# Kernel tuning notes

Measured on AMD Instinct MI355X. Metric: run time of the kernel, lower is better.

## Reference

```python
import jax, jax.numpy as jnp
import numpy as np
import math

_KX = np.array([[1., 0., -1.], [2., 0., -2.], [1., 0., -1.]], dtype=np.float32)
_SOBEL = np.stack([_KX, _KX.T])[:, None]  # (2,1,3,3): gx, gy
_SCALES = [16, 8, 4, 2, 1]
_NBINS = 9


def _hog_layer(x, pw, pb, pool):
    # x: (B,1,H,W); reflect-pad 3x3 Sobel conv -> (B,2,H,W)
    xp = jnp.pad(x, ((0, 0), (0, 0), (1, 1), (1, 1)), mode='reflect')
    gxy = jax.lax.conv_general_dilated(
        xp, jnp.asarray(_SOBEL), (1, 1), 'VALID',
        dimension_numbers=('NCHW', 'OIHW', 'NCHW'))
    gx, gy = gxy[:, 0], gxy[:, 1]
    mag = jnp.sqrt(gx * gx + gy * gy)                       # (B,H,W)
    phase = jnp.arctan2(gx, gy)
    bins = (jnp.floor(phase / math.pi * _NBINS) % _NBINS).astype(jnp.int32)
    # one-hot scatter of magnitude into orientation bins (matches scatter_ on dim 1)
    out = jax.nn.one_hot(bins, _NBINS, dtype=mag.dtype) * mag[..., None]  # (B,H,W,9)
    out = jnp.transpose(out, (0, 3, 1, 2))                  # (B,9,H,W)
    # 1x1 conv with stride=pool == strided slice + channel mix
    o = out[:, :, ::pool, ::pool]
    h = jnp.einsum('oc,nchw->nohw', pw, o) + pb[None, :, None, None]
    nrm = jnp.linalg.norm(h, axis=1, keepdims=True)
    return h / jnp.maximum(nrm, 1e-12)                      # F.normalize(p=2, dim=1)


def _hog_rgb(imgs, pw, pb, pool):
    # run the (shared) HOG layer on R,G,B independently, concat on channel dim
    N, C, H, W = imgs.shape
    h = _hog_layer(imgs.reshape(N * C, 1, H, W), pw, pb, pool)
    return h.reshape(N, C * _NBINS, h.shape[2], h.shape[3])  # (N,27,H/s,W/s)


def _recal_mask(mask, s):
    B, H, W = mask.shape[0], mask.shape[2], mask.shape[3]
    m = mask.astype(jnp.float32).reshape(B, H // s, s, W // s, s)
    return jnp.transpose(m, (0, 1, 3, 2, 4)).mean((-2, -1))  # (B,H/s,W/s)


def _loss(preds, imgs, mask, pws, pbs):
    loss = jnp.float32(0.0)
    for k, s in enumerate(_SCALES):
        tgt = _hog_rgb(imgs, pws[k], pbs[k], s)
        M = _recal_mask(mask, s)
        loss = loss + (((preds[k] - tgt) ** 2).mean(axis=1) * M).sum() / M.sum()
    return loss


def setup_inputs() -> dict:
    key = jax.random.key(0)
    ks = jax.random.split(key, 20)
    N, H, W = 32, 224, 224
    d = {}
    d['imgs'] = jax.random.normal(ks[0], (N, 3, H, W), dtype=jnp.float32)
    d['mask'] = jax.random.uniform(ks[1], (N, 1, H, W), dtype=jnp.float32)
    for k, s in enumerate(_SCALES):
        d['pred%d' % k] = jax.random.normal(ks[2 + k], (N, 27, H // s, W // s), dtype=jnp.float32)
        d['pw%d' % k] = jax.random.normal(ks[7 + k], (9, 9), dtype=jnp.float32) / 3.0
        d['pb%d' % k] = jax.random.normal(ks[12 + k], (9,), dtype=jnp.float32) / 3.0
    return d


def reference(imgs, mask, pred0, pred1, pred2, pred3, pred4,
              pw0, pw1, pw2, pw3, pw4, pb0, pb1, pb2, pb3, pb4):
    preds = [pred0, pred1, pred2, pred3, pred4]
    pws = [pw0, pw1, pw2, pw3, pw4]
    pbs = [pb0, pb1, pb2, pb3, pb4]
    return _loss(preds, imgs, mask, pws, pbs)
```

## Files before the change

kernel.cpp:

```cpp
#include <hip/hip_runtime.h>

#define N_IMG 32
#define H_IMG 224
#define W_IMG 224

#define BS16_END 25
#define BS8_END 123
#define BS4_END 515
#define BS2_END 2083
#define NBLK_TOTAL 8355

__device__ __forceinline__ int reflect_idx(int i, int n) {
    if (i < 0) return -i;
    if (i >= n) return 2 * n - 2 - i;
    return i;
}

__device__ __forceinline__ int bin_from_g(float gx, float gy) {
    float u = gx * __builtin_copysignf(1.0f, gy);
    float w = __builtin_fabsf(gy);
    const float T[9] = {-5.6712818f, -1.7320508f, -0.83909963f, -0.36397023f,
                        0.0f, 0.36397023f, 0.83909963f, 1.7320508f, 5.6712818f};
    int c = 0;
    #pragma unroll
    for (int k = 0; k < 9; ++k) c += (u >= T[k] * w) ? 1 : 0;
    int b = c + 4;
    return (b >= 9) ? b - 9 : b;
}

template <int S>
__device__ __forceinline__ void scale_body(int rel_bid,
    const float* __restrict__ imgs, const float* __restrict__ mask,
    const float* __restrict__ pred,
    const float* spwT, const float* spb, const float* sA, const float* sB,
    float Cc, float& local, float& mlocal)
{
    constexpr int Hs = H_IMG / S, Ws = W_IMG / S;
    int vt = rel_bid * 256 + (int)threadIdx.x;
    if (vt >= N_IMG * Hs * Ws) return;
    int j = vt % Ws;
    int t = vt / Ws;
    int i = t % Hs;
    int n = t / Hs;

    float M;
    const float* mbase = mask + (size_t)n * H_IMG * W_IMG + (size_t)(i * S) * W_IMG + j * S;
    if constexpr (S == 1) {
        M = mbase[0];
    } else if constexpr (S == 2) {
        float2 a = *(const float2*)(mbase);
        float2 b = *(const float2*)(mbase + W_IMG);
        M = (a.x + a.y + b.x + b.y) * 0.25f;
    } else {
        float msum = 0.0f;
        #pragma unroll
        for (int a = 0; a < S; ++a) {
            const float* mr = mbase + (size_t)a * W_IMG;
            #pragma unroll
            for (int q = 0; q < S / 4; ++q) {
                float4 fv = *(const float4*)(mr + q * 4);
                msum += (fv.x + fv.y) + (fv.z + fv.w);
            }
        }
        M = msum * (1.0f / (float)(S * S));
    }

    int y = i * S, x = j * S;
    int y0 = reflect_idx(y - 1, H_IMG), y2 = reflect_idx(y + 1, H_IMG);
    int x0 = reflect_idx(x - 1, W_IMG), x2 = reflect_idx(x + 1, W_IMG);
    constexpr size_t cstride = (size_t)Hs * Ws;

    float d2 = 0.0f;
    #pragma unroll
    for (int c = 0; c < 3; ++c) {
        const float* im = imgs + (size_t)(n * 3 + c) * H_IMG * W_IMG;
        const float* q0 = im + (size_t)y0 * W_IMG;
        const float* q1 = im + (size_t)y  * W_IMG;
        const float* q2 = im + (size_t)y2 * W_IMG;
        float p00 = q0[x0], p01 = q0[x], p02 = q0[x2];
        float p10 = q1[x0],             p12 = q1[x2];
        float p20 = q2[x0], p21 = q2[x], p22 = q2[x2];

        const float* pr = pred + ((size_t)(n * 27 + c * 9) * Hs + i) * Ws + j;
        float p[9];
        #pragma unroll
        for (int o = 0; o < 9; ++o) p[o] = pr[o * cstride];

        float gx = (p00 - p02) + 2.0f * (p10 - p12) + (p20 - p22);
        float gy = (p00 - p20) + 2.0f * (p01 - p21) + (p02 - p22);
        float mag = sqrtf(gx * gx + gy * gy);
        int bn = bin_from_g(gx, gy);
        float nrm2 = fmaf(mag, fmaf(mag, sA[bn], 2.0f * sB[bn]), Cc);
        float inv = 1.0f / fmaxf(sqrtf(nrm2), 1e-12f);

        #pragma unroll
        for (int o = 0; o < 9; ++o) {
            float h = fmaf(spwT[bn * 9 + o], mag, spb[o]) * inv;
            float dd = p[o] - h;
            d2 += dd * dd;
        }
    }

    local = M * d2 * (1.0f / 27.0f);
    if constexpr (S == 1) mlocal = M;
}

__global__ void __launch_bounds__(256) fused_kernel(
    const float* __restrict__ imgs, const float* __restrict__ mask,
    const float* __restrict__ pred0, const float* __restrict__ pred1,
    const float* __restrict__ pred2, const float* __restrict__ pred3,
    const float* __restrict__ pred4,
    const float* __restrict__ pw0, const float* __restrict__ pw1,
    const float* __restrict__ pw2, const float* __restrict__ pw3,
    const float* __restrict__ pw4,
    const float* __restrict__ pb0, const float* __restrict__ pb1,
    const float* __restrict__ pb2, const float* __restrict__ pb3,
    const float* __restrict__ pb4,
    double* __restrict__ pl, double* __restrict__ pm)
{
    __shared__ float spwT[81];
    __shared__ float spb[9];
    __shared__ float sA[9], sB[9], sC[1];

    int bid = blockIdx.x;
    const float* pw;  const float* pb;
    if (bid < BS16_END)      { pw = pw0; pb = pb0; }
    else if (bid < BS8_END)  { pw = pw1; pb = pb1; }
    else if (bid < BS4_END)  { pw = pw2; pb = pb2; }
    else if (bid < BS2_END)  { pw = pw3; pb = pb3; }
    else                     { pw = pw4; pb = pb4; }

    if (threadIdx.x < 81) {
        int o = threadIdx.x / 9, b = threadIdx.x % 9;
        spwT[b * 9 + o] = pw[threadIdx.x];
    }
    if (threadIdx.x < 9) spb[threadIdx.x] = pb[threadIdx.x];
    __syncthreads();
    if (threadIdx.x < 9) {
        float A = 0.0f, B = 0.0f;
        #pragma unroll
        for (int o = 0; o < 9; ++o) {
            float w = spwT[threadIdx.x * 9 + o];
            A += w * w;
            B += w * spb[o];
        }
        sA[threadIdx.x] = A;
        sB[threadIdx.x] = B;
        if (threadIdx.x == 0) {
            float Cc = 0.0f;
            #pragma unroll
            for (int o = 0; o < 9; ++o) Cc += spb[o] * spb[o];
            sC[0] = Cc;
        }
    }
    __syncthreads();
    float Cc = sC[0];

    float local = 0.0f, mlocal = 0.0f;
    if (bid < BS16_END)      scale_body<16>(bid,            imgs, mask, pred0, spwT, spb, sA, sB, Cc, local, mlocal);
    else if (bid < BS8_END)  scale_body<8>(bid - BS16_END,  imgs, mask, pred1, spwT, spb, sA, sB, Cc, local, mlocal);
    else if (bid < BS4_END)  scale_body<4>(bid - BS8_END,   imgs, mask, pred2, spwT, spb, sA, sB, Cc, local, mlocal);
    else if (bid < BS2_END)  scale_body<2>(bid - BS4_END,   imgs, mask, pred3, spwT, spb, sA, sB, Cc, local, mlocal);
    else                     scale_body<1>(bid - BS2_END,   imgs, mask, pred4, spwT, spb, sA, sB, Cc, local, mlocal);

    #pragma unroll
    for (int off = 32; off > 0; off >>= 1) {
        local  += __shfl_down(local,  off, 64);
        mlocal += __shfl_down(mlocal, off, 64);
    }
    __shared__ float s1[4], s2[4];
    int lane = threadIdx.x & 63, wid = threadIdx.x >> 6;
    if (lane == 0) { s1[wid] = local; s2[wid] = mlocal; }
    __syncthreads();
    if (threadIdx.x == 0) {
        pl[bid] = (double)(s1[0] + s1[1] + s1[2] + s1[3]);
        pm[bid] = (double)(s2[0] + s2[1] + s2[2] + s2[3]);
    }
}

__global__ void __launch_bounds__(256) finalize_kernel(
    const double* __restrict__ pl, const double* __restrict__ pm,
    float* __restrict__ out)
{
    double l = 0.0, m = 0.0;
    for (int idx = threadIdx.x; idx < NBLK_TOTAL; idx += 256) {
        double w = (idx < BS16_END) ? 256.0 : (idx < BS8_END) ? 64.0
                 : (idx < BS4_END) ? 16.0 : (idx < BS2_END) ? 4.0 : 1.0;
        l += w * pl[idx];
        m += pm[idx];
    }
    #pragma unroll
    for (int off = 32; off > 0; off >>= 1) {
        l += __shfl_down(l, off, 64);
        m += __shfl_down(m, off, 64);
    }
    __shared__ double sl[4], sm[4];
    int lane = threadIdx.x & 63, wid = threadIdx.x >> 6;
    if (lane == 0) { sl[wid] = l; sm[wid] = m; }
    __syncthreads();
    if (threadIdx.x == 0)
        out[0] = (float)((sl[0] + sl[1] + sl[2] + sl[3]) / (sm[0] + sm[1] + sm[2] + sm[3]));
}

extern "C" void kernel_launch(void* const* d_in, const int* in_sizes, int n_in,
                              void* d_out, int out_size, void* d_ws, size_t ws_size,
                              hipStream_t stream) {
    (void)in_sizes; (void)n_in; (void)out_size; (void)ws_size;
    const float* imgs = (const float*)d_in[0];
    const float* mask = (const float*)d_in[1];
    const float* pred[5];
    const float* pw[5];
    const float* pb[5];
    for (int k = 0; k < 5; ++k) {
        pred[k] = (const float*)d_in[2 + 3 * k];
        pw[k]   = (const float*)d_in[3 + 3 * k];
        pb[k]   = (const float*)d_in[4 + 3 * k];
    }
    double* pl = (double*)d_ws;
    double* pm = pl + NBLK_TOTAL;

    fused_kernel<<<NBLK_TOTAL, 256, 0, stream>>>(
        imgs, mask,
        pred[0], pred[1], pred[2], pred[3], pred[4],
        pw[0], pw[1], pw[2], pw[3], pw[4],
        pb[0], pb[1], pb[2], pb[3], pb[4],
        pl, pm);
    finalize_kernel<<<1, 256, 0, stream>>>(pl, pm, (float*)d_out);
}
```

Before: 71.69 us.

## Tile full-resolution scale by 4-row slabs with shared per-pixel gradient stats and prefetch

Switches to 512-thread blocks. For scale 1, each block now handles a 4-row slab of one image. It first computes the gradient magnitude, bin and normalization for all three channels into shared memory using float4 image loads. It then streams the 27 prediction planes with float4 loads and register double-buffering, so the per-pixel gradient work is done once rather than being tied to per-thread scattered 9-plane reads. Scale weights move into the fused kernel, which simplifies finalize, at the cost of more shared memory and more complex indexing.

New measurement: 105.2 us. +46.7%, slower.

```diff
diff --git a/kernel.cpp b/kernel.cpp
--- a/kernel.cpp
+++ b/kernel.cpp
@@ -3,12 +3,14 @@
 #define N_IMG 32
 #define H_IMG 224
 #define W_IMG 224
-
-#define BS16_END 25
-#define BS8_END 123
-#define BS4_END 515
-#define BS2_END 2083
-#define NBLK_TOTAL 8355
+#define HW 50176
+
+#define BS16_END 13
+#define BS8_END 62
+#define BS4_END 258
+#define BS2_END 1042
+#define NBLK_TOTAL 2834
+#define NTHR 512
 
 __device__ __forceinline__ int reflect_idx(int i, int n) {
     if (i < 0) return -i;
@@ -29,25 +31,22 @@
 }
 
 template <int S>
-__device__ __forceinline__ void scale_body(int rel_bid,
+__device__ __forceinline__ float scale_unit(int vt,
     const float* __restrict__ imgs, const float* __restrict__ mask,
     const float* __restrict__ pred,
     const float* spwT, const float* spb, const float* sA, const float* sB,
-    float Cc, float& local, float& mlocal)
+    float Cc)
 {
     constexpr int Hs = H_IMG / S, Ws = W_IMG / S;
-    int vt = rel_bid * 256 + (int)threadIdx.x;
-    if (vt >= N_IMG * Hs * Ws) return;
+    if (vt >= N_IMG * Hs * Ws) return 0.0f;
     int j = vt % Ws;
     int t = vt / Ws;
     int i = t % Hs;
     int n = t / Hs;
 
     float M;
-    const float* mbase = mask + (size_t)n * H_IMG * W_IMG + (size_t)(i * S) * W_IMG + j * S;
-    if constexpr (S == 1) {
-        M = mbase[0];
-    } else if constexpr (S == 2) {
+    const float* mbase = mask + (size_t)n * HW + (size_t)(i * S) * W_IMG + j * S;
+    if constexpr (S == 2) {
         float2 a = *(const float2*)(mbase);
         float2 b = *(const float2*)(mbase + W_IMG);
         M = (a.x + a.y + b.x + b.y) * 0.25f;
@@ -73,7 +72,7 @@
     float d2 = 0.0f;
     #pragma unroll
     for (int c = 0; c < 3; ++c) {
-        const float* im = imgs + (size_t)(n * 3 + c) * H_IMG * W_IMG;
+        const float* im = imgs + (size_t)(n * 3 + c) * HW;
         const float* q0 = im + (size_t)y0 * W_IMG;
         const float* q1 = im + (size_t)y  * W_IMG;
         const float* q2 = im + (size_t)y2 * W_IMG;
@@ -101,11 +100,10 @@
         }
     }
 
-    local = M * d2 * (1.0f / 27.0f);
-    if constexpr (S == 1) mlocal = M;
-}
-
-__global__ void __launch_bounds__(256) fused_kernel(
+    return M * d2 * (1.0f / 27.0f);
+}
+
+__global__ void __launch_bounds__(NTHR) fused_kernel(
     const float* __restrict__ imgs, const float* __restrict__ mask,
     const float* __restrict__ pred0, const float* __restrict__ pred1,
     const float* __restrict__ pred2, const float* __restrict__ pred3,
@@ -121,8 +119,14 @@
     __shared__ float spwT[81];
     __shared__ float spb[9];
     __shared__ float sA[9], sB[9], sC[1];
+    __shared__ float sminv[3 * 4 * 4 * 56];
+    __shared__ float sinvv[3 * 4 * 4 * 56];
+    __shared__ unsigned char sbinv[3 * 4 * 4 * 56];
+    __shared__ float smask[4 * 4 * 56];
 
     int bid = blockIdx.x;
+    int tid = (int)threadIdx.x;
+
     const float* pw;  const float* pb;
     if (bid < BS16_END)      { pw = pw0; pb = pb0; }
     else if (bid < BS8_END)  { pw = pw1; pb = pb1; }
@@ -130,51 +134,150 @@
     else if (bid < BS2_END)  { pw = pw3; pb = pb3; }
     else                     { pw = pw4; pb = pb4; }
 
-    if (threadIdx.x < 81) {
-        int o = threadIdx.x / 9, b = threadIdx.x % 9;
-        spwT[b * 9 + o] = pw[threadIdx.x];
-    }
-    if (threadIdx.x < 9) spb[threadIdx.x] = pb[threadIdx.x];
+    if (tid < 81) {
+        int o = tid / 9, b = tid % 9;
+        spwT[b * 9 + o] = pw[tid];
+    }
+    if (tid < 9) spb[tid] = pb[tid];
     __syncthreads();
-    if (threadIdx.x < 9) {
+    if (tid < 9) {
         float A = 0.0f, B = 0.0f;
         #pragma unroll
         for (int o = 0; o < 9; ++o) {
-            float w = spwT[threadIdx.x * 9 + o];
+            float w = spwT[tid * 9 + o];
             A += w * w;
             B += w * spb[o];
         }
-        sA[threadIdx.x] = A;
-        sB[threadIdx.x] = B;
-        if (threadIdx.x == 0) {
-            float Cc = 0.0f;
+        sA[tid] = A;
+        sB[tid] = B;
+        if (tid == 0) {
+            float Cv = 0.0f;
             #pragma unroll
-            for (int o = 0; o < 9; ++o) Cc += spb[o] * spb[o];
-            sC[0] = Cc;
+            for (int o = 0; o < 9; ++o) Cv += spb[o] * spb[o];
+            sC[0] = Cv;
         }
     }
     __syncthreads();
     float Cc = sC[0];
 
-    float local = 0.0f, mlocal = 0.0f;
-    if (bid < BS16_END)      scale_body<16>(bid,            imgs, mask, pred0, spwT, spb, sA, sB, Cc, local, mlocal);
-    else if (bid < BS8_END)  scale_body<8>(bid - BS16_END,  imgs, mask, pred1, spwT, spb, sA, sB, Cc, local, mlocal);
-    else if (bid < BS4_END)  scale_body<4>(bid - BS8_END,   imgs, mask, pred2, spwT, spb, sA, sB, Cc, local, mlocal);
-    else if (bid < BS2_END)  scale_body<2>(bid - BS4_END,   imgs, mask, pred3, spwT, spb, sA, sB, Cc, local, mlocal);
-    else                     scale_body<1>(bid - BS2_END,   imgs, mask, pred4, spwT, spb, sA, sB, Cc, local, mlocal);
+    float lacc = 0.0f, macc = 0.0f;
+
+    if (bid < BS2_END) {
+        if (bid < BS16_END)
+            lacc = 256.0f * scale_unit<16>(bid * NTHR + tid, imgs, mask, pred0, spwT, spb, sA, sB, Cc);
+        else if (bid < BS8_END)
+            lacc = 64.0f * scale_unit<8>((bid - BS16_END) * NTHR + tid, imgs, mask, pred1, spwT, spb, sA, sB, Cc);
+        else if (bid < BS4_END)
+            lacc = 16.0f * scale_unit<4>((bid - BS8_END) * NTHR + tid, imgs, mask, pred2, spwT, spb, sA, sB, Cc);
+        else
+            lacc = 4.0f * scale_unit<2>((bid - BS4_END) * NTHR + tid, imgs, mask, pred3, spwT, spb, sA, sB, Cc);
+    } else {
+        int rel  = bid - BS2_END;
+        int n    = rel / 56;
+        int slab = rel % 56;
+        int r0   = slab * 4;
+
+        for (int u = tid; u < 672; u += NTHR) {
+            int c   = u / 224;
+            int rem = u % 224;
+            int r   = rem / 56;
+            int jv  = rem % 56;
+            int j0  = jv * 4;
+            int gi  = r0 + r;
+            int y0 = reflect_idx(gi - 1, H_IMG), y2 = reflect_idx(gi + 1, H_IMG);
+            int xl = reflect_idx(j0 - 1, W_IMG), xr = reflect_idx(j0 + 4, W_IMG);
+            const float* im = imgs + (size_t)(n * 3 + c) * HW;
+            const float* q0 = im + (size_t)y0 * W_IMG;
+            const float* q1 = im + (size_t)gi * W_IMG;
+            const float* q2 = im + (size_t)y2 * W_IMG;
+            float a0[6], a1[6], a2[6];
+            float4 f;
+            a0[0] = q0[xl]; f = *(const float4*)(q0 + j0);
+            a0[1] = f.x; a0[2] = f.y; a0[3] = f.z; a0[4] = f.w; a0[5] = q0[xr];
+            a1[0] = q1[xl]; f = *(const float4*)(q1 + j0);
+            a1[1] = f.x; a1[2] = f.y; a1[3] = f.z; a1[4] = f.w; a1[5] = q1[xr];
+            a2[0] = q2[xl]; f = *(const float4*)(q2 + j0);
+            a2[1] = f.x; a2[2] = f.y; a2[3] = f.z; a2[4] = f.w; a2[5] = q2[xr];
+            int base = (c * 4 + r) * 4;
+            #pragma unroll
+            for (int e = 0; e < 4; ++e) {
+                float gx = (a0[e] - a0[e + 2]) + 2.0f * (a1[e] - a1[e + 2]) + (a2[e] - a2[e + 2]);
+                float gy = (a0[e] - a2[e]) + 2.0f * (a0[e + 1] - a2[e + 1]) + (a0[e + 2] - a2[e + 2]);
+                float mag = sqrtf(gx * gx + gy * gy);
+                int bn = bin_from_g(gx, gy);
+                float nrm2 = fmaf(mag, fmaf(mag, sA[bn], 2.0f * sB[bn]), Cc);
+                float inv = 1.0f / fmaxf(sqrtf(nrm2), 1e-12f);
+                int li = (base + e) * 56 + jv;
+                sminv[li] = mag * inv;
+                sinvv[li] = inv;
+                sbinv[li] = (unsigned char)bn;
+            }
+        }
+        if (tid < 224) {
+            int r = tid / 56, jv = tid % 56;
+            const float* mb = mask + (size_t)n * HW + (size_t)r0 * W_IMG + tid * 4;
+            float4 mv = *(const float4*)mb;
+            float me[4] = {mv.x, mv.y, mv.z, mv.w};
+            #pragma unroll
+            for (int e = 0; e < 4; ++e) smask[(r * 4 + e) * 56 + jv] = me[e];
+            macc = (me[0] + me[1]) + (me[2] + me[3]);
+        }
+        __syncthreads();
+
+        const float* pbase = pred4 + (size_t)(n * 27) * HW + (size_t)r0 * W_IMG;
+        int idx = tid;
+        float4 cur;
+        if (idx < 6048) {
+            int p = idx / 224, off = idx % 224;
+            cur = *(const float4*)(pbase + (size_t)p * HW + off * 4);
+        }
+        while (idx < 6048) {
+            int nidx = idx + NTHR;
+            float4 nxt;
+            if (nidx < 6048) {
+                int p = nidx / 224, off = nidx % 224;
+                nxt = *(const float4*)(pbase + (size_t)p * HW + off * 4);
+            }
+            {
+                int p = idx / 224, off = idx % 224;
+                int c = p / 9, o = p % 9;
+                int r = off / 56, jv = off % 56;
+                float wrow = 0.0f;
+                float pbo = spb[o];
+                float pe[4] = {cur.x, cur.y, cur.z, cur.w};
+                int cb = (c * 4 + r) * 4;
+                int mb = r * 4;
+                #pragma unroll
+                for (int e = 0; e < 4; ++e) {
+                    int li = (cb + e) * 56 + jv;
+                    int bn = (int)sbinv[li];
+                    float h = fmaf(spwT[bn * 9 + o], sminv[li], pbo * sinvv[li]);
+                    float dd = pe[e] - h;
+                    wrow = fmaf(smask[(mb + e) * 56 + jv] * dd, dd, wrow);
+                }
+                lacc += wrow;
+            }
+            cur = nxt;
+            idx = nidx;
+        }
+        lacc *= (1.0f / 27.0f);
+    }
 
     #pragma unroll
     for (int off = 32; off > 0; off >>= 1) {
-        local  += __shfl_down(local,  off, 64);
-        mlocal += __shfl_down(mlocal, off, 64);
-    }
-    __shared__ float s1[4], s2[4];
-    int lane = threadIdx.x & 63, wid = threadIdx.x >> 6;
-    if (lane == 0) { s1[wid] = local; s2[wid] = mlocal; }
+        lacc += __shfl_down(lacc, off, 64);
+        macc += __shfl_down(macc, off, 64);
+    }
+    __shared__ float red1[8], red2[8];
+    int lane = tid & 63, wid = tid >> 6;
+    if (lane == 0) { red1[wid] = lacc; red2[wid] = macc; }
     __syncthreads();
-    if (threadIdx.x == 0) {
-        pl[bid] = (double)(s1[0] + s1[1] + s1[2] + s1[3]);
-        pm[bid] = (double)(s2[0] + s2[1] + s2[2] + s2[3]);
+    if (tid == 0) {
+        float l = 0.0f, m = 0.0f;
+        #pragma unroll
+        for (int w = 0; w < 8; ++w) { l += red1[w]; m += red2[w]; }
+        pl[bid] = (double)l;
+        pm[bid] = (double)m;
     }
 }
 
@@ -184,9 +287,7 @@
 {
     double l = 0.0, m = 0.0;
     for (int idx = threadIdx.x; idx < NBLK_TOTAL; idx += 256) {
-        double w = (idx < BS16_END) ? 256.0 : (idx < BS8_END) ? 64.0
-                 : (idx < BS4_END) ? 16.0 : (idx < BS2_END) ? 4.0 : 1.0;
-        l += w * pl[idx];
+        l += pl[idx];
         m += pm[idx];
     }
     #pragma unroll
@@ -219,7 +320,7 @@
     double* pl = (double*)d_ws;
     double* pm = pl + NBLK_TOTAL;
 
-    fused_kernel<<<NBLK_TOTAL, 256, 0, stream>>>(
+    fused_kernel<<<NBLK_TOTAL, NTHR, 0, stream>>>(
         imgs, mask,
         pred[0], pred[1], pred[2], pred[3], pred[4],
         pw[0], pw[1], pw[2], pw[3], pw[4],
```
